# Kernel tuning notes

Hardware: AMD Instinct MI355X
Metric: run time of the kernel (lower is better)

## Reference

```python
import jax, jax.numpy as jnp
import numpy as np

NUM_HEADS = 12

def setup_inputs() -> dict:
    key = jax.random.key(0)
    k1, k2, k3, k4 = jax.random.split(key, 4)
    B, N, D = 8, 1024, 768
    x = jax.random.normal(k1, (B, N, D), dtype=jnp.float32)
    mask = jax.random.randint(k2, (B, N), 0, 2, dtype=jnp.int32)
    Wqkv = jax.random.normal(k3, (3 * D, D), dtype=jnp.float32) * (D ** -0.5)
    Wproj = jax.random.normal(k4, (D, D), dtype=jnp.float32) * (D ** -0.5)
    bproj = jnp.zeros((D,), dtype=jnp.float32)
    return {"x": x, "mask": mask, "Wqkv": Wqkv, "Wproj": Wproj, "bproj": bproj}

def reference(x, mask, Wqkv, Wproj, bproj):
    B, N, D = x.shape
    H = NUM_HEADS
    hd = D // H
    scale = hd ** -0.5
    # QKV projection (no bias), split into q,k,v of shape [B,H,N,hd]
    qkv = jnp.einsum('bnd,ed->bne', x, Wqkv).reshape(B, N, 3, H, hd)
    qkv = jnp.transpose(qkv, (2, 0, 3, 1, 4))
    q, k, v = qkv[0], qkv[1], qkv[2]
    # padding mask: attend where both query and key are valid; masked-out
    # (padded) query rows attend only to themselves (diagonal) to avoid NaNs
    m = mask.astype(bool)  # [B,N]
    pair = m[:, None, :, None] & m[:, None, None, :]          # [B,1,N,N]
    diag = jnp.eye(N, dtype=bool)[None, None]                 # [1,1,N,N]
    attn_mask = pair | (diag & ~m[:, None, :, None])          # [B,1,N,N]
    scores = jnp.einsum('bhnd,bhmd->bhnm', q, k) * scale      # [B,H,N,N]
    scores = jnp.where(attn_mask, scores, jnp.finfo(scores.dtype).min)
    attn = jax.nn.softmax(scores, axis=-1)
    out = jnp.einsum('bhnm,bhmd->bhnd', attn, v)
    out = jnp.transpose(out, (0, 2, 1, 3)).reshape(B, N, D)
    out = jnp.einsum('bnd,ed->bne', out, Wproj) + bproj
    return out
```

## Files before the change

kernel.cpp:

```cpp
#include <hip/hip_runtime.h>
#include <hip/hip_bf16.h>
#include <stdint.h>


typedef unsigned short u16;
typedef __attribute__((ext_vector_type(8))) short short8;
typedef __attribute__((ext_vector_type(4))) float f32x4;

#define MFMA16(a, b, c) __builtin_amdgcn_mfma_f32_16x16x32_bf16((a), (b), (c), 0, 0, 0)

static __device__ __forceinline__ u16 f2bf(float f) {
    __hip_bfloat16 h = __float2bfloat16(f);
    return *(u16*)&h;
}
static __device__ __forceinline__ void gld16(const u16* g, u16* l) {
  __builtin_amdgcn_global_load_lds(
      (const __attribute__((address_space(1))) void*)g,
      (__attribute__((address_space(3))) void*)l, 16, 0, 0);
}

__global__ __launch_bounds__(256) void cvt_bf16(
    const float* __restrict__ s0, u16* __restrict__ d0, int n0,
    const float* __restrict__ s1, u16* __restrict__ d1, int n1,
    const float* __restrict__ s2, u16* __restrict__ d2, int n2) {
  int i = (blockIdx.x * 256 + threadIdx.x) * 4;
  const float* s; u16* d;
  if (i < n0) { s = s0 + i; d = d0 + i; }
  else if ((i -= n0) < n1) { s = s1 + i; d = d1 + i; }
  else if ((i -= n1) < n2) { s = s2 + i; d = d2 + i; }
  else return;
  float4 v = *(const float4*)s;
  ushort4 o;
  o.x = f2bf(v.x); o.y = f2bf(v.y); o.z = f2bf(v.z); o.w = f2bf(v.w);
  *(ushort4*)d = o;
}

template<int K, int BN, int LDC, bool BF16OUT>
__global__ __launch_bounds__(256) void gemm_bt(
    const u16* __restrict__ A,
    const u16* __restrict__ B,
    void* __restrict__ Cout,
    const float* __restrict__ bias) {
  constexpr int NT = BN / 32;
  __shared__ u16 As[128 * 32];
  __shared__ u16 Bs[BN * 32];
  const int tid = threadIdx.x;
  const int w = tid >> 6, l = tid & 63;
  const int lane16 = l & 15, quad = l >> 4;
  const int i0 = blockIdx.y * 128, j0 = blockIdx.x * BN;
  const int mh = (w & 1) * 64;
  const int nh = (w >> 1) * (BN / 2);

  f32x4 acc[4][NT];
  #pragma unroll
  for (int mt = 0; mt < 4; mt++)
    #pragma unroll
    for (int nt = 0; nt < NT; nt++) acc[mt][nt] = (f32x4){0.f, 0.f, 0.f, 0.f};

  for (int kt = 0; kt < K / 32; kt++) {
    const int k0 = kt * 32;
    __syncthreads();
    #pragma unroll
    for (int s = 0; s < 2; s++) {
      int idx = tid + s * 256;
      int row = idx >> 2, c8 = (idx & 3) * 8;
      gld16(&A[(size_t)(i0 + row) * K + k0 + c8], &As[idx * 8]);
    }
    #pragma unroll
    for (int s = 0; s < BN / 64; s++) {
      int idx = tid + s * 256;
      int row = idx >> 2, c8 = (idx & 3) * 8;
      gld16(&B[(size_t)(j0 + row) * K + k0 + c8], &Bs[idx * 8]);
    }
    __syncthreads();

    short8 af[4], bf[NT];
    #pragma unroll
    for (int mt = 0; mt < 4; mt++)
      af[mt] = *(const short8*)&As[(mh + mt * 16 + lane16) * 32 + quad * 8];
    #pragma unroll
    for (int nt = 0; nt < NT; nt++)
      bf[nt] = *(const short8*)&Bs[(nh + nt * 16 + lane16) * 32 + quad * 8];
    #pragma unroll
    for (int mt = 0; mt < 4; mt++)
      #pragma unroll
      for (int nt = 0; nt < NT; nt++)
        acc[mt][nt] = MFMA16(af[mt], bf[nt], acc[mt][nt]);
  }

  #pragma unroll
  for (int mt = 0; mt < 4; mt++) {
    #pragma unroll
    for (int nt = 0; nt < NT; nt++) {
      int col = j0 + nh + nt * 16 + lane16;
      #pragma unroll
      for (int r = 0; r < 4; r++) {
        int row = i0 + mh + mt * 16 + quad * 4 + r;
        if (BF16OUT) {
          ((u16*)Cout)[(size_t)row * LDC + col] = f2bf(acc[mt][nt][r]);
        } else {
          ((float*)Cout)[(size_t)row * LDC + col] = acc[mt][nt][r] + bias[col];
        }
      }
    }
  }
}

__global__ __launch_bounds__(256, 3) void attn_mfma(
    const u16* __restrict__ qkv,
    const int* __restrict__ mask,
    u16* __restrict__ ctx) {
  __shared__ u16 Ks[64][72];
  __shared__ u16 Vt[64][72];
  __shared__ u16 Ps[4][32][72];
  __shared__ float mkb[64];
  __shared__ int mqs[128];

  const int tid = threadIdx.x;
  const int w = tid >> 6, l = tid & 63;
  const int lane16 = l & 15, quad = l >> 4;
  const int idx = blockIdx.x;
  const int bh = idx % 96;
  const int rb = idx / 96;
  const int b = bh / 12, h = bh % 12;
  const int n0 = rb * 128;
  const int baseRow = b * 1024;

  const int key_s = tid >> 2, ds_s = (tid & 3) * 16;
  const int kA_s = (tid & 31) * 2, dg_s = tid >> 5;

  if (tid < 128) mqs[tid] = mask[baseRow + n0 + tid];

  short8 qfrag[2][2];
  #pragma unroll
  for (int qt = 0; qt < 2; qt++) {
    const u16* qp = qkv + (size_t)(baseRow + n0 + w*32 + qt*16 + lane16) * 2304 + h*64;
    #pragma unroll
    for (int ks = 0; ks < 2; ks++)
      qfrag[qt][ks] = *(const short8*)(qp + ks*32 + quad*8);
  }

  f32x4 oacc[2][4];
  #pragma unroll
  for (int qt = 0; qt < 2; qt++)
    #pragma unroll
    for (int nt = 0; nt < 4; nt++) oacc[qt][nt] = (f32x4){0.f, 0.f, 0.f, 0.f};
  f32x4 lsum4[2] = {(f32x4){0.f,0.f,0.f,0.f}, (f32x4){0.f,0.f,0.f,0.f}};

  const float K1 = 0.18033688011112043f;
  const float K0 = -23.083120654223415f;

  uint4 kr0, kr1, vr0, vr1;
  int mraw = 0;
  {
    const u16* kp = qkv + (size_t)(baseRow + key_s) * 2304 + 768 + h*64 + ds_s;
    kr0 = *(const uint4*)kp;
    kr1 = *(const uint4*)(kp + 8);
    const u16* vp = qkv + (size_t)(baseRow + kA_s) * 2304 + 1536 + h*64 + dg_s*8;
    vr0 = *(const uint4*)vp;
    vr1 = *(const uint4*)(vp + 2304);
    if (tid < 64) mraw = mask[baseRow + tid];
  }

  for (int c = 0; c < 16; c++) {
    if (c) __syncthreads();

    *(uint4*)&Ks[key_s][ds_s]     = kr0;
    *(uint4*)&Ks[key_s][ds_s + 8] = kr1;
    {
      const u16* va = (const u16*)&vr0;
      const u16* vb = (const u16*)&vr1;
      #pragma unroll
      for (int j = 0; j < 8; j++)
        *(unsigned int*)&Vt[dg_s*8 + j][kA_s] =
            (unsigned int)va[j] | ((unsigned int)vb[j] << 16);
      if (tid < 64) mkb[tid] = mraw ? 0.f : -1e38f;
    }

    if (c + 1 < 16) {
      const u16* kp = qkv + (size_t)(baseRow + (c+1)*64 + key_s) * 2304 + 768 + h*64 + ds_s;
      kr0 = *(const uint4*)kp;
      kr1 = *(const uint4*)(kp + 8);
      const u16* vp = qkv + (size_t)(baseRow + (c+1)*64 + kA_s) * 2304 + 1536 + h*64 + dg_s*8;
      vr0 = *(const uint4*)vp;
      vr1 = *(const uint4*)(vp + 2304);
      if (tid < 64) mraw = mask[baseRow + (c+1)*64 + tid];
    }
    __syncthreads();

    f32x4 sacc[4][2];
    #pragma unroll
    for (int kt = 0; kt < 4; kt++)
      #pragma unroll
      for (int qt = 0; qt < 2; qt++) sacc[kt][qt] = (f32x4){0.f, 0.f, 0.f, 0.f};
    #pragma unroll
    for (int ks = 0; ks < 2; ks++) {
      short8 kf[4];
      #pragma unroll
      for (int kt = 0; kt < 4; kt++)
        kf[kt] = *(const short8*)&Ks[kt*16 + lane16][ks*32 + quad*8];
      __builtin_amdgcn_s_setprio(1);
      #pragma unroll
      for (int kt = 0; kt < 4; kt++)
        #pragma unroll
        for (int qt = 0; qt < 2; qt++)
          sacc[kt][qt] = MFMA16(kf[kt], qfrag[qt][ks], sacc[kt][qt]);
      __builtin_amdgcn_s_setprio(0);
    }

    #pragma unroll
    for (int kt = 0; kt < 4; kt++) {
      f32x4 mk4 = *(const f32x4*)&mkb[kt*16 + quad*4];
      #pragma unroll
      for (int qt = 0; qt < 2; qt++) {
        u16 pk[4];
        #pragma unroll
        for (int r = 0; r < 4; r++) {
          float e = __builtin_amdgcn_exp2f(fmaf(sacc[kt][qt][r], K1, K0) + mk4[r]);
          lsum4[qt][r] += e;
          pk[r] = f2bf(e);
        }
        uint2 pv;
        pv.x = (unsigned int)pk[0] | ((unsigned int)pk[1] << 16);
        pv.y = (unsigned int)pk[2] | ((unsigned int)pk[3] << 16);
        *(uint2*)&Ps[w][qt*16 + lane16][kt*16 + quad*4] = pv;
      }
    }

    #pragma unroll
    for (int kc = 0; kc < 2; kc++) {
      short8 pf[2], vf[4];
      #pragma unroll
      for (int qt = 0; qt < 2; qt++)
        pf[qt] = *(const short8*)&Ps[w][qt*16 + lane16][kc*32 + quad*8];
      #pragma unroll
      for (int nt = 0; nt < 4; nt++)
        vf[nt] = *(const short8*)&Vt[nt*16 + lane16][kc*32 + quad*8];
      __builtin_amdgcn_s_setprio(1);
      #pragma unroll
      for (int qt = 0; qt < 2; qt++)
        #pragma unroll
        for (int nt = 0; nt < 4; nt++)
          oacc[qt][nt] = MFMA16(pf[qt], vf[nt], oacc[qt][nt]);
      __builtin_amdgcn_s_setprio(0);
    }
  }

  float linv[2][4];
  #pragma unroll
  for (int qt = 0; qt < 2; qt++) {
    float s = lsum4[qt][0] + lsum4[qt][1] + lsum4[qt][2] + lsum4[qt][3];
    s += __shfl_xor(s, 16);
    s += __shfl_xor(s, 32);
    #pragma unroll
    for (int r = 0; r < 4; r++)
      linv[qt][r] = 1.0f / __shfl(s, quad*4 + r);
  }
  #pragma unroll
  for (int qt = 0; qt < 2; qt++) {
    #pragma unroll
    for (int r = 0; r < 4; r++) {
      int rl = w*32 + qt*16 + quad*4 + r;
      int rg = n0 + rl;
      int mq = mqs[rl];
      #pragma unroll
      for (int nt = 0; nt < 4; nt++) {
        u16 outv;
        if (mq) {
          outv = f2bf(oacc[qt][nt][r] * linv[qt][r]);
        } else {
          outv = qkv[(size_t)(baseRow + rg) * 2304 + 1536 + h*64 + nt*16 + lane16];
        }
        ctx[(size_t)(baseRow + rg) * 768 + h*64 + nt*16 + lane16] = outv;
      }
    }
  }
}

extern "C" void kernel_launch(void* const* d_in, const int* in_sizes, int n_in,
                              void* d_out, int out_size, void* d_ws, size_t ws_size,
                              hipStream_t stream) {
  const float* x     = (const float*)d_in[0];
  const int*   mask  = (const int*)d_in[1];
  const float* Wqkv  = (const float*)d_in[2];
  const float* Wproj = (const float*)d_in[3];
  const float* bproj = (const float*)d_in[4];
  float* out = (float*)d_out;

  const int NX = 8192 * 768;
  const int NQ = 2304 * 768;
  const int NP = 768 * 768;

  char* wsb = (char*)d_ws;
  u16* qkv    = (u16*)wsb;
  u16* ctx    = (u16*)(wsb + (size_t)8192 * 2304 * 2);
  u16* xb     = (u16*)(wsb + (size_t)8192 * 2304 * 2 + (size_t)8192 * 768 * 2);
  u16* wqkvb  = xb + NX;
  u16* wprojb = wqkvb + NQ;

  int cvt_blocks = ((NX + NQ + NP) / 4 + 255) / 256;
  cvt_bf16<<<dim3(cvt_blocks), 256, 0, stream>>>(x, xb, NX, Wqkv, wqkvb, NQ, Wproj, wprojb, NP);

  gemm_bt<768, 128, 2304, true><<<dim3(18, 64), 256, 0, stream>>>(xb, wqkvb, qkv, nullptr);
  attn_mfma<<<dim3(768), 256, 0, stream>>>(qkv, mask, ctx);
  gemm_bt<768, 64, 768, false><<<dim3(12, 64), 256, 0, stream>>>(ctx, wprojb, out, bproj);
}
```

Measured before the change: 198.1 us.

## Remap GEMM blocks per XCD and preload full key mask into LDS

The GEMM grid becomes 1D, and block indices are remapped so each group of blocks dispatched round-robin to the same XCD covers a contiguous range of output tiles. This is meant to improve L2 reuse of the A and B tiles on the multi-XCD MI355X. The attention kernel now loads the whole 1024-entry mask row once as float biases into LDS, removing the per-chunk mask loads and LDS writes inside the loop. The cost is 4KB more LDS per block, which may affect occupancy.

```diff
diff --git a/kernel.cpp b/kernel.cpp
--- a/kernel.cpp
+++ b/kernel.cpp
@@ -35,7 +35,7 @@
   *(ushort4*)d = o;
 }
 
-template<int K, int BN, int LDC, bool BF16OUT>
+template<int K, int BN, int LDC, bool BF16OUT, int NXB>
 __global__ __launch_bounds__(256) void gemm_bt(
     const u16* __restrict__ A,
     const u16* __restrict__ B,
@@ -47,7 +47,13 @@
   const int tid = threadIdx.x;
   const int w = tid >> 6, l = tid & 63;
   const int lane16 = l & 15, quad = l >> 4;
-  const int i0 = blockIdx.y * 128, j0 = blockIdx.x * BN;
+
+  constexpr int nwg = NXB * 64;
+  constexpr int qch = nwg / 8;
+  const int orig = blockIdx.x;
+  const int logical = (orig & 7) * qch + (orig >> 3);
+  const int i0 = (logical / NXB) * 128, j0 = (logical % NXB) * BN;
+
   const int mh = (w & 1) * 64;
   const int nh = (w >> 1) * (BN / 2);
 
@@ -113,8 +119,7 @@
   __shared__ u16 Ks[64][72];
   __shared__ u16 Vt[64][72];
   __shared__ u16 Ps[4][32][72];
-  __shared__ float mkb[64];
-  __shared__ int mqs[128];
+  __shared__ float mkb_all[1024];
 
   const int tid = threadIdx.x;
   const int w = tid >> 6, l = tid & 63;
@@ -129,7 +134,15 @@
   const int key_s = tid >> 2, ds_s = (tid & 3) * 16;
   const int kA_s = (tid & 31) * 2, dg_s = tid >> 5;
 
-  if (tid < 128) mqs[tid] = mask[baseRow + n0 + tid];
+  {
+    int4 mv = *(const int4*)&mask[baseRow + tid * 4];
+    f32x4 mf;
+    mf[0] = mv.x ? 0.f : -1e38f;
+    mf[1] = mv.y ? 0.f : -1e38f;
+    mf[2] = mv.z ? 0.f : -1e38f;
+    mf[3] = mv.w ? 0.f : -1e38f;
+    *(f32x4*)&mkb_all[tid * 4] = mf;
+  }
 
   short8 qfrag[2][2];
   #pragma unroll
@@ -151,7 +164,6 @@
   const float K0 = -23.083120654223415f;
 
   uint4 kr0, kr1, vr0, vr1;
-  int mraw = 0;
   {
     const u16* kp = qkv + (size_t)(baseRow + key_s) * 2304 + 768 + h*64 + ds_s;
     kr0 = *(const uint4*)kp;
@@ -159,7 +171,6 @@
     const u16* vp = qkv + (size_t)(baseRow + kA_s) * 2304 + 1536 + h*64 + dg_s*8;
     vr0 = *(const uint4*)vp;
     vr1 = *(const uint4*)(vp + 2304);
-    if (tid < 64) mraw = mask[baseRow + tid];
   }
 
   for (int c = 0; c < 16; c++) {
@@ -174,7 +185,6 @@
       for (int j = 0; j < 8; j++)
         *(unsigned int*)&Vt[dg_s*8 + j][kA_s] =
             (unsigned int)va[j] | ((unsigned int)vb[j] << 16);
-      if (tid < 64) mkb[tid] = mraw ? 0.f : -1e38f;
     }
 
     if (c + 1 < 16) {
@@ -184,7 +194,6 @@
       const u16* vp = qkv + (size_t)(baseRow + (c+1)*64 + kA_s) * 2304 + 1536 + h*64 + dg_s*8;
       vr0 = *(const uint4*)vp;
       vr1 = *(const uint4*)(vp + 2304);
-      if (tid < 64) mraw = mask[baseRow + (c+1)*64 + tid];
     }
     __syncthreads();
 
@@ -210,7 +219,7 @@
 
     #pragma unroll
     for (int kt = 0; kt < 4; kt++) {
-      f32x4 mk4 = *(const f32x4*)&mkb[kt*16 + quad*4];
+      f32x4 mk4 = *(const f32x4*)&mkb_all[c*64 + kt*16 + quad*4];
       #pragma unroll
       for (int qt = 0; qt < 2; qt++) {
         u16 pk[4];
@@ -262,7 +271,7 @@
     for (int r = 0; r < 4; r++) {
       int rl = w*32 + qt*16 + quad*4 + r;
       int rg = n0 + rl;
-      int mq = mqs[rl];
+      int mq = (mkb_all[n0 + rl] == 0.f);
       #pragma unroll
       for (int nt = 0; nt < 4; nt++) {
         u16 outv;
@@ -301,7 +310,7 @@
   int cvt_blocks = ((NX + NQ + NP) / 4 + 255) / 256;
   cvt_bf16<<<dim3(cvt_blocks), 256, 0, stream>>>(x, xb, NX, Wqkv, wqkvb, NQ, Wproj, wprojb, NP);
 
-  gemm_bt<768, 128, 2304, true><<<dim3(18, 64), 256, 0, stream>>>(xb, wqkvb, qkv, nullptr);
+  gemm_bt<768, 128, 2304, true, 18><<<dim3(18 * 64), 256, 0, stream>>>(xb, wqkvb, qkv, nullptr);
   attn_mfma<<<dim3(768), 256, 0, stream>>>(qkv, mask, ctx);
-  gemm_bt<768, 64, 768, false><<<dim3(12, 64), 256, 0, stream>>>(ctx, wprojb, out, bproj);
-}
+  gemm_bt<768, 64, 768, false, 12><<<dim3(12 * 64), 256, 0, stream>>>(ctx, wprojb, out, bproj);
+}
```

Result: faster. 191.5 us (-3.4%).
